# Kernel tuning notes

Measured on AMD Instinct MI355X. Metric: run time of the kernel, lower is better.

Reference implementation:

```python
import jax, jax.numpy as jnp
import numpy as np

B, S, C, H, W = 8, 20, 512, 48, 48
KC, VC, OC = 256, 512, 512

def conv1x1(x, w, b):
    # x: (B, Cin, H, W), w: (Cout, Cin), b: (Cout,)
    return jnp.einsum('oc,bchw->bohw', w, x) + b[None, :, None, None]

def setup_inputs() -> dict:
    key = jax.random.key(0)
    ks = jax.random.split(key, 16)
    sc = lambda cin: 1.0 / np.sqrt(cin)
    return {
        'key': jax.random.normal(ks[0], (B, C, H, W), jnp.float32),
        'query': jax.random.normal(ks[1], (B, S, C), jnp.float32),
        'word_id': jax.random.randint(ks[2], (B, S), 0, 1000),
        'wv_w': jax.random.normal(ks[3], (C, C), jnp.float32) * sc(C),
        'wv_b': jnp.zeros((C,), jnp.float32),
        'fk_w': jax.random.normal(ks[4], (KC, C), jnp.float32) * sc(C),
        'fk_b': jnp.zeros((KC,), jnp.float32),
        'fq_w': jax.random.normal(ks[5], (KC, C), jnp.float32) * sc(C),
        'fq_b': jnp.zeros((KC,), jnp.float32),
        'fv_w': jax.random.normal(ks[6], (VC, C), jnp.float32) * sc(C),
        'fv_b': jnp.zeros((VC,), jnp.float32),
        'w1_w': jax.random.normal(ks[7], (OC, 2 * C), jnp.float32) * sc(2 * C),
        'w1_b': jnp.zeros((OC,), jnp.float32),
        'w2_w': jax.random.normal(ks[8], (OC, C), jnp.float32) * sc(C),
        'w2_b': jnp.zeros((OC,), jnp.float32),
    }

def reference(key, query, word_id, wv_w, wv_b, fk_w, fk_b, fq_w, fq_b,
              fv_w, fv_b, w1_w, w1_b, w2_w, w2_b):
    b, c, h, w = key.shape
    hw = h * w
    # --- WordVisualAttention: context=query (B,S,C), visual=key ---
    vis = conv1x1(key, wv_w, wv_b).reshape(b, c, hw)          # (B,C,HW)
    attn = jnp.einsum('bsc,bcn->bsn', query, vis)             # (B,S,HW)
    attn = jax.nn.softmax(attn, axis=1)                       # softmax over seq dim
    mask = (word_id != 0).astype(attn.dtype)[:, :, None]      # (B,S,1)
    attn = attn * mask
    attn = attn / jnp.sum(attn, axis=1, keepdims=True)
    wemb = jnp.einsum('bsc,bsn->bcn', query, attn).reshape(b, c, h, w)
    # --- non-local cross attention ---
    k = conv1x1(key, fk_w, fk_b).reshape(b, KC, hw)           # (B,KC,HW)
    q = conv1x1(wemb, fq_w, fq_b).reshape(b, KC, hw)
    v = conv1x1(key, fv_w, fv_b).reshape(b, VC, hw)
    sim = jnp.einsum('bkn,bkm->bnm', q, k) * (KC ** -0.5)     # (B,HW,HW)
    sim = jax.nn.softmax(sim, axis=-1)
    ctx = jnp.einsum('bnm,bcm->bcn', sim, v).reshape(b, VC, h, w)
    out1 = conv1x1(jnp.concatenate([ctx, wemb], axis=1), w1_w, w1_b)
    out2 = conv1x1(ctx, w2_w, w2_b) + out1
    return out2
```

## Files before the change

### kernel.cpp

```cpp
#include <hip/hip_runtime.h>

#define NHW 2304
#define NB  8
#define NS  20
#define NC  512
#define SCL 0.09016844005555897f

typedef unsigned short u16;
typedef unsigned char u8;
typedef short short8 __attribute__((ext_vector_type(8)));
typedef unsigned short u16x8 __attribute__((ext_vector_type(8)));
typedef u8 u8x16 __attribute__((ext_vector_type(16)));
typedef float f32x4 __attribute__((ext_vector_type(4)));

__device__ __forceinline__ float b2f(u16 u) {
    unsigned int v = ((unsigned int)u) << 16;
    return __builtin_bit_cast(float, v);
}
__device__ __forceinline__ u16 f2b(float f) {
    unsigned int u = __builtin_bit_cast(unsigned int, f);
    u += 0x7fffu + ((u >> 16) & 1u);
    return (u16)(u >> 16);
}

__device__ __forceinline__ u8 f2e4_sw(float f) {
    unsigned int u = __builtin_bit_cast(unsigned int, f);
    u8 sign = (u >> 24) & 0x80;
    unsigned int a = u & 0x7FFFFFFFu;
    if (a >= 0x43E00000u) return sign | 0x7E;
    int e = (int)(a >> 23) - 127;
    unsigned int m = (a & 0x7FFFFF) | 0x800000;
    int ne = e + 7;
    if (ne <= 0) {
        int shift = 21 - ne;
        if (shift > 24) return sign;
        unsigned int q = m >> shift;
        unsigned int rem = m & ((1u << shift) - 1);
        unsigned int half = 1u << (shift - 1);
        q += (rem > half) || (rem == half && (q & 1));
        return sign | (u8)q;
    }
    unsigned int q = m >> 20;
    unsigned int rem = m & 0xFFFFFu;
    q += (rem > 0x80000u) || (rem == 0x80000u && (q & 1));
    if (q >= 16) { q >>= 1; ne++; }
    if (ne >= 16 || (ne == 15 && q == 15)) return sign | 0x7E;
    return sign | (u8)((ne << 3) | (q & 7));
}
__device__ __forceinline__ float e42f_sw(u8 v) {
    int e = (v >> 3) & 15;
    int m = v & 7;
    float r;
    if (e == 0) r = (float)m * 0.001953125f;
    else {
        unsigned int bits = ((unsigned int)(e + 120) << 23) | ((unsigned int)m << 20);
        r = __builtin_bit_cast(float, bits);
    }
    return (v & 0x80) ? -r : r;
}

#if defined(__has_builtin)
#if __has_builtin(__builtin_amdgcn_cvt_pk_fp8_f32) && __has_builtin(__builtin_amdgcn_cvt_f32_fp8)
#define HW_FP8 1
#endif
#endif

template<bool HI>
__device__ __forceinline__ unsigned int pk2_fp8(float a, float b, unsigned int old) {
#ifdef HW_FP8
    return (unsigned int)__builtin_amdgcn_cvt_pk_fp8_f32(a, b, (int)old, HI);
#else
    unsigned int lo = (unsigned int)f2e4_sw(a) | ((unsigned int)f2e4_sw(b) << 8);
    return HI ? ((old & 0x0000FFFFu) | (lo << 16)) : ((old & 0xFFFF0000u) | lo);
#endif
}
#ifdef HW_FP8
#define DEC_FP8(w, sel) __builtin_amdgcn_cvt_f32_fp8((int)(w), (sel))
#else
#define DEC_FP8(w, sel) e42f_sw((u8)((w) >> (8 * (sel))))
#endif

__device__ __forceinline__ void load_lds16(const void* g, void* l) {
    __builtin_amdgcn_global_load_lds((const __attribute__((address_space(1))) void*)g,
                                     (__attribute__((address_space(3))) void*)l, 16, 0, 0);
}

__global__ __launch_bounds__(256)
void gemm_nt_bf16(const u16* __restrict__ A, long As, int lda,
                  const u16* __restrict__ B, long Bs, int ldb,
                  void* __restrict__ C, long Cs, int ldc,
                  int K, const float* __restrict__ bias, int bias_mode,
                  float scale, int out_mode)
{
    __shared__ __align__(16) u16 sA[2 * 4096];
    __shared__ __align__(16) u16 sB[2 * 4096];
    const int tid   = threadIdx.x;
    const int b     = blockIdx.z;
    const int nBase = blockIdx.x * 128;
    const int mBase = blockIdx.y * 128;
    const u16* Ab = A + (size_t)b * As + (size_t)mBase * lda;
    const u16* Bb = B + (size_t)b * Bs + (size_t)nBase * ldb;
    const int lane = tid & 63;
    const int wave = tid >> 6;
    const int wr = wave >> 1, wc = wave & 1;
    const int srow[4] = { ((wave * 4 + 0) & 7) * 16 + (lane >> 2),
                          ((wave * 4 + 1) & 7) * 16 + (lane >> 2),
                          ((wave * 4 + 2) & 7) * 16 + (lane >> 2),
                          ((wave * 4 + 3) & 7) * 16 + (lane >> 2) };
    const int swzw = ((lane & 3) ^ ((lane >> 3) & 3)) * 8;
    const int rsw  = ((lane >> 4) ^ ((lane >> 1) & 3)) * 8;
    f32x4 acc[4][4] = {};
    for (int k0 = 0; k0 < K; k0 += 64) {
        __syncthreads();
        #pragma unroll
        for (int it = 0; it < 4; ++it) {
            const int chunk = wave * 4 + it;
            const int kofs = (chunk >> 3) * 32 + swzw;
            load_lds16(&Ab[(size_t)srow[it] * lda + k0 + kofs], &sA[chunk * 512 + lane * 8]);
            load_lds16(&Bb[(size_t)srow[it] * ldb + k0 + kofs], &sB[chunk * 512 + lane * 8]);
        }
        __syncthreads();
        #pragma unroll
        for (int kk = 0; kk < 2; ++kk) {
            short8 af[4], bg[4];
            #pragma unroll
            for (int i = 0; i < 4; ++i)
                af[i] = *(const short8*)&sA[kk * 4096 + (wr * 64 + i * 16 + (lane & 15)) * 32 + rsw];
            #pragma unroll
            for (int j = 0; j < 4; ++j)
                bg[j] = *(const short8*)&sB[kk * 4096 + (wc * 64 + j * 16 + (lane & 15)) * 32 + rsw];
            #pragma unroll
            for (int i = 0; i < 4; ++i)
                #pragma unroll
                for (int j = 0; j < 4; ++j)
                    acc[i][j] = __builtin_amdgcn_mfma_f32_16x16x32_bf16(af[i], bg[j], acc[i][j], 0, 0, 0);
        }
    }
    const int r0 = mBase + wr * 64 + (lane >> 4) * 4;
    const int c0 = nBase + wc * 64 + (lane & 15);
    #pragma unroll
    for (int i = 0; i < 4; ++i) {
        #pragma unroll
        for (int r = 0; r < 4; ++r) {
            const int row = r0 + i * 16 + r;
            const float br = (bias_mode == 1) ? bias[row] : 0.f;
            if (out_mode == 2) {
                float vv[4];
                #pragma unroll
                for (int j = 0; j < 4; ++j) vv[j] = acc[i][j][r] * scale + br;
                unsigned int w = 0;
                w = pk2_fp8<false>(vv[0], vv[1], w);
                w = pk2_fp8<true>(vv[2], vv[3], w);
                #pragma unroll
                for (int j = 0; j < 4; ++j)
                    ((u8*)C)[(size_t)b * Cs + (size_t)row * ldc + c0 + j * 16] = (u8)(w >> (8 * j));
            } else {
                #pragma unroll
                for (int j = 0; j < 4; ++j) {
                    const int col = c0 + j * 16;
                    float v = acc[i][j][r] * scale + br;
                    const size_t off = (size_t)b * Cs + (size_t)row * ldc + col;
                    if (out_mode == 1) ((float*)C)[off] = v;
                    else               ((u16*)C)[off] = f2b(v);
                }
            }
        }
    }
}

__global__ __launch_bounds__(256)
void e_gemm(const u16* __restrict__ attnwT, const u16* __restrict__ ks,
            u8* __restrict__ E8, float* __restrict__ Dpart)
{
    __shared__ __align__(16) u16 sA[128 * 32];
    __shared__ __align__(16) u16 sB[128 * 32];
    __shared__ __align__(16) u8 Etile[128 * 128];
    __shared__ float Dsh[2][128];
    const int tid = threadIdx.x;
    const int b = blockIdx.z;
    const int mt = blockIdx.x, nt = blockIdx.y;
    const int mBase = mt * 128, nBase = nt * 128;
    const u16* Ab = attnwT + ((size_t)b * NHW + nBase) * 32;
    const u16* Bb = ks     + ((size_t)b * NHW + mBase) * 32;
    const int lane = tid & 63;
    const int wave = tid >> 6;
    const int wr = wave >> 1, wc = wave & 1;
    const int str = tid >> 2;
    const int stk = (tid & 3) * 8;
    load_lds16(&Ab[(size_t)str * 32 + stk],        &sA[tid * 8]);
    load_lds16(&Ab[(size_t)(str + 64) * 32 + stk], &sA[2048 + tid * 8]);
    load_lds16(&Bb[(size_t)str * 32 + stk],        &sB[tid * 8]);
    load_lds16(&Bb[(size_t)(str + 64) * 32 + stk], &sB[2048 + tid * 8]);
    __syncthreads();
    short8 af[4], bg[4];
    #pragma unroll
    for (int i = 0; i < 4; ++i)
        af[i] = *(const short8*)&sA[(wr * 64 + i * 16 + (lane & 15)) * 32 + (lane >> 4) * 8];
    #pragma unroll
    for (int j = 0; j < 4; ++j)
        bg[j] = *(const short8*)&sB[(wc * 64 + j * 16 + (lane & 15)) * 32 + (lane >> 4) * 8];
    f32x4 acc[4][4] = {};
    #pragma unroll
    for (int i = 0; i < 4; ++i)
        #pragma unroll
        for (int j = 0; j < 4; ++j)
            acc[i][j] = __builtin_amdgcn_mfma_f32_16x16x32_bf16(af[i], bg[j], acc[i][j], 0, 0, 0);

    float dpart[16] = {};
    #pragma unroll
    for (int i = 0; i < 4; ++i) {
        #pragma unroll
        for (int r = 0; r < 4; ++r) {
            const int rowloc = wr * 64 + i * 16 + (lane >> 4) * 4 + r;
            unsigned int w = 0;
            w = pk2_fp8<false>(exp2f(acc[i][0][r]), exp2f(acc[i][1][r]), w);
            w = pk2_fp8<true>(exp2f(acc[i][2][r]), exp2f(acc[i][3][r]), w);
            dpart[i * 4 + r] += DEC_FP8(w, 0) + DEC_FP8(w, 1) + DEC_FP8(w, 2) + DEC_FP8(w, 3);
            #pragma unroll
            for (int j = 0; j < 4; ++j) {
                const int colloc = wc * 64 + j * 16 + (lane & 15);
                Etile[rowloc * 128 + (colloc ^ ((rowloc & 7) << 4))] = (u8)(w >> (8 * j));
            }
        }
    }
    #pragma unroll
    for (int mask = 1; mask < 16; mask <<= 1)
        #pragma unroll
        for (int k = 0; k < 16; ++k)
            dpart[k] += __shfl_xor(dpart[k], mask, 64);
    if ((lane & 15) == 0) {
        #pragma unroll
        for (int i = 0; i < 4; ++i)
            #pragma unroll
            for (int r = 0; r < 4; ++r)
                Dsh[wc][wr * 64 + i * 16 + (lane >> 4) * 4 + r] = dpart[i * 4 + r];
    }
    __syncthreads();
    if (tid < 128)
        Dpart[((size_t)(b * 18 + mt)) * NHW + nBase + tid] = Dsh[0][tid] + Dsh[1][tid];
    #pragma unroll
    for (int rep = 0; rep < 4; ++rep) {
        const int row = wave * 32 + rep * 8 + (lane >> 3);
        const int slot = lane & 7;
        u8x16 v = *(const u8x16*)&Etile[row * 128 + ((slot ^ (row & 7)) << 4)];
        *(u8x16*)&E8[((size_t)b * NHW + nBase + row) * NHW + mBase + slot * 16] = v;
    }
}

__global__ __launch_bounds__(256)
void pv_gemm(const u8* __restrict__ vp8, const u8* __restrict__ E8,
             const float* __restrict__ Dpart, const float* __restrict__ attnw,
             const float* __restrict__ Ofold, const float* __restrict__ b2,
             float* __restrict__ out)
{
    __shared__ __align__(16) u8 sA[16384];
    __shared__ __align__(16) u8 sB[16384];
    __shared__ float DsumSh[128];
    __shared__ float DinvSh[128];
    const int tid = threadIdx.x;
    const int bid = blockIdx.x;
    const int xcd = bid & 7, slot = bid >> 3;
    const int b = xcd;
    const int nt = slot >> 2;
    const int ot = slot & 3;
    const int oBase = ot * 128, nBase = nt * 128;

    const u8* A8 = vp8 + ((size_t)b * NC + oBase) * NHW;
    const u8* B8 = E8  + ((size_t)b * NHW + nBase) * NHW;
    const int lane = tid & 63;
    const int wave = tid >> 6;
    const int wr = wave >> 1, wc = wave & 1;

    int srowS[4], sgofS[4];
    #pragma unroll
    for (int it = 0; it < 4; ++it) {
        const int cd = (wave * 4 + it) * 64 + lane;
        srowS[it] = cd >> 3;
        sgofS[it] = ((cd & 7) ^ ((cd >> 3) & 7)) * 16;
    }
    #define PV_STAGE(k0) { \
        _Pragma("unroll") \
        for (int it = 0; it < 4; ++it) { \
            load_lds16(&A8[(size_t)srowS[it] * NHW + (k0) + sgofS[it]], &sA[((wave * 4 + it) * 64 + lane) * 16]); \
            load_lds16(&B8[(size_t)srowS[it] * NHW + (k0) + sgofS[it]], &sB[((wave * 4 + it) * 64 + lane) * 16]); \
        } }

    u16* sAh = (u16*)sA;
    u16* sBh = (u16*)sB;
    if (tid < 128) {
        float s = 0.f;
        #pragma unroll
        for (int mt = 0; mt < 18; ++mt)
            s += Dpart[((size_t)(b * 18 + mt)) * NHW + nBase + tid];
        DsumSh[tid] = s;
        DinvSh[tid] = 1.f / s;
    }
    for (int idx = tid; idx < 128 * 32; idx += 256) {
        const int o = idx >> 5, s = idx & 31;
        float v = 0.f;
        if (s < 20) v = Ofold[((size_t)b * 768 + 256 + oBase + o) * NS + s];
        else if (s == 20) v = b2[oBase + o];
        sAh[idx] = f2b(v);
    }
    __syncthreads();
    for (int idx = tid; idx < 128 * 32; idx += 256) {
        const int n = idx >> 5, s = idx & 31;
        float v = 0.f;
        if (s <= 20) {
            const float ds = DsumSh[n];
            v = (s < 20) ? attnw[((size_t)b * NS + s) * NHW + nBase + n] * ds : ds;
        }
        sBh[idx] = f2b(v);
    }
    __syncthreads();

    f32x4 acc[4][4];
    {
        const f32x4 zero = {0.f, 0.f, 0.f, 0.f};
        short8 qf[4], afr[4];
        #pragma unroll
        for (int i = 0; i < 4; ++i)
            qf[i] = *(const short8*)&sAh[(wr * 64 + i * 16 + (lane & 15)) * 32 + (lane >> 4) * 8];
        #pragma unroll
        for (int j = 0; j < 4; ++j)
            afr[j] = *(const short8*)&sBh[(wc * 64 + j * 16 + (lane & 15)) * 32 + (lane >> 4) * 8];
        #pragma unroll
        for (int i = 0; i < 4; ++i)
            #pragma unroll
            for (int j = 0; j < 4; ++j)
                acc[i][j] = __builtin_amdgcn_mfma_f32_16x16x32_bf16(qf[i], afr[j], zero, 0, 0, 0);
    }

    const int krow_a = wr * 64 + (lane & 15);
    const int krow_b = wc * 64 + (lane & 15);
    const int khalf = ((lane >> 4) & 1) * 8;
    const int kc2   = (lane >> 5);

    for (int k0 = 0; k0 < NHW; k0 += 128) {
        __syncthreads();
        PV_STAGE(k0);
        __syncthreads();
        #pragma unroll
        for (int kk = 0; kk < 4; ++kk) {
            long af[4], bg[4];
            #pragma unroll
            for (int i = 0; i < 4; ++i) {
                const int row = krow_a + i * 16;
                const int c = (kk * 2 + kc2) ^ (row & 7);
                af[i] = *(const long*)&sA[row * 128 + c * 16 + khalf];
            }
            #pragma unroll
            for (int j = 0; j < 4; ++j) {
                const int row = krow_b + j * 16;
                const int c = (kk * 2 + kc2) ^ (row & 7);
                bg[j] = *(const long*)&sB[row * 128 + c * 16 + khalf];
            }
            #pragma unroll
            for (int i = 0; i < 4; ++i)
                #pragma unroll
                for (int j = 0; j < 4; ++j)
                    acc[i][j] = __builtin_amdgcn_mfma_f32_16x16x32_fp8_fp8(af[i], bg[j], acc[i][j], 0, 0, 0);
        }
    }
    #pragma unroll
    for (int i = 0; i < 4; ++i) {
        #pragma unroll
        for (int r = 0; r < 4; ++r) {
            const int rowloc = wr * 64 + i * 16 + (lane >> 4) * 4 + r;
            #pragma unroll
            for (int j = 0; j < 4; ++j) {
                const int colloc = wc * 64 + j * 16 + (lane & 15);
                out[((size_t)b * NC + oBase + rowloc) * NHW + nBase + colloc] =
                    acc[i][j][r] * DinvSh[colloc];
            }
        }
    }
    #undef PV_STAGE
}

__global__ __launch_bounds__(256)
void prep_all(const float* __restrict__ key, u16* __restrict__ keyT,
              const float* __restrict__ fv_w, u16* __restrict__ fvT,
              const float* __restrict__ w1, const float* __restrict__ w1b,
              const float* __restrict__ w2, const float* __restrict__ w2b,
              const float* __restrict__ fvb, u16* __restrict__ wc2b,
              float* __restrict__ b2,
              const float* __restrict__ query, const float* __restrict__ wv_w,
              const float* __restrict__ wv_b, float* __restrict__ qw,
              float* __restrict__ qb,
              const float* __restrict__ fq, float* __restrict__ O)
{
    __shared__ __align__(16) char smem[44032];
    const int bid = blockIdx.x;
    const int tid = threadIdx.x;

    if (bid < 2368) {
        const float* src; u16* dst; int R, Cc, cBase, rBase, b;
        if (bid < 2304) {
            src = key; dst = keyT; R = NC; Cc = NHW;
            cBase = (bid % 36) * 64; rBase = ((bid / 36) % 8) * 64; b = bid / 288;
        } else {
            const int t2 = bid - 2304;
            src = fv_w; dst = fvT; R = 512; Cc = 512;
            cBase = (t2 % 8) * 64; rBase = (t2 / 8) * 64; b = 0;
        }
        u16 (*t)[72] = (u16(*)[72])smem;
        const float* sb = src + ((size_t)b * R + rBase) * Cc + cBase;
        const int ln = tid & 63;
        const int lr = tid >> 6;
        #pragma unroll
        for (int rr = 0; rr < 16; ++rr) {
            int r = lr + rr * 4;
            t[r][ln] = f2b(sb[(size_t)r * Cc + ln]);
        }
        __syncthreads();
        u16* ob = dst + ((size_t)b * Cc + cBase) * R + rBase;
        #pragma unroll
        for (int rep = 0; rep < 2; ++rep) {
            int slot = rep * 256 + tid;
            int cc = slot >> 3;
            int r8 = (slot & 7) * 8;
            u16x8 v;
            #pragma unroll
            for (int e = 0; e < 8; ++e) v[e] = t[r8 + e][cc];
            *(u16x8*)&ob[(size_t)cc * R + r8] = v;
        }
    } else if (bid < 2880) {
        const int o = bid - 2368;
        float* red = (float*)smem;
        float part = 0.f;
        for (int c = tid; c < 512; c += 256) {
            float v = w1[(size_t)o * 1024 + c] + w2[(size_t)o * 512 + c];
            wc2b[(size_t)o * 512 + c] = f2b(v);
            part += v * fvb[c];
        }
        #pragma unroll
        for (int off = 32; off > 0; off >>= 1) part += __shfl_down(part, off, 64);
        if ((tid & 63) == 0) red[tid >> 6] = part;
        __syncthreads();
        if (tid == 0) b2[o] = (red[0] + red[1]) + (red[2] + red[3]) + w1b[o] + w2b[o];
    } else if (bid < 3040) {
        const int t3 = bid - 2880;
        const int s = t3 % NS, b = t3 / NS;
        float* qs  = (float*)smem;
        float* red = qs + 512;
        qs[tid] = query[((size_t)b * NS + s) * NC + tid];
        qs[tid + 256] = query[((size_t)b * NS + s) * NC + tid + 256];
        __syncthreads();
        float a0 = 0.f, a1 = 0.f;
        for (int o = 0; o < NC; ++o) {
            float qv = qs[o];
            a0 += qv * wv_w[(size_t)o * NC + tid];
            a1 += qv * wv_w[(size_t)o * NC + tid + 256];
        }
        qw[((size_t)b * NS + s) * NC + tid] = a0;
        qw[((size_t)b * NS + s) * NC + tid + 256] = a1;
        float pb = qs[tid] * wv_b[tid] + qs[tid + 256] * wv_b[tid + 256];
        #pragma unroll
        for (int off = 32; off > 0; off >>= 1) pb += __shfl_down(pb, off, 64);
        if ((tid & 63) == 0) red[tid >> 6] = pb;
        __syncthreads();
        if (tid == 0) qb[b * NS + s] = (red[0] + red[1]) + (red[2] + red[3]);
    } else {
        const int t4 = bid - 3040;
        const int x = t4 % 48, b = t4 / 48;
        float (*qsh)[NC] = (float(*)[NC])smem;
        for (int idx = tid; idx < NS * NC; idx += 256)
            qsh[idx >> 9][idx & 511] = query[(size_t)b * NS * NC + idx];
        __syncthreads();
        const int row = x * 16 + (tid >> 4);
        const int ct = tid & 15;
        const float* wp = (row < 256) ? &fq[(size_t)row * NC]
                                      : &w1[(size_t)(row - 256) * 1024 + 512];
        float acc[NS] = {};
        #pragma unroll 4
        for (int i = 0; i < 32; ++i) {
            int c = ct + i * 16;
            float w = wp[c];
            #pragma unroll
            for (int s = 0; s < NS; ++s) acc[s] += w * qsh[s][c];
        }
        #pragma unroll
        for (int off = 1; off < 16; off <<= 1)
            #pragma unroll
            for (int s = 0; s < NS; ++s) acc[s] += __shfl_xor(acc[s], off, 64);
        if (ct == 0) {
            #pragma unroll
            for (int s = 0; s < NS; ++s)
                O[((size_t)b * 768 + row) * NS + s] = acc[s];
        }
    }
}

__global__ __launch_bounds__(256)
void scan_wk(const float* __restrict__ key, const float* __restrict__ qw,
             const float* __restrict__ qb, const int* __restrict__ wid,
             const float* __restrict__ g, const float* __restrict__ h,
             float* __restrict__ attnw, u16* __restrict__ attnwT,
             u16* __restrict__ ks)
{
    __shared__ float qshT[NC][20];
    __shared__ u16 gshb[NC][22];
    __shared__ float red[3][64][7];
    __shared__ float msk[20], qbs[20], hsh[21];
    const int b = blockIdx.y;
    const int tid = threadIdx.x;
    const float* qwb = qw + (size_t)b * NS * NC;
    for (int idx = tid; idx < NC * 20; idx += 256) {
        int c = idx / 20, s = idx - c * 20;
        qshT[c][s] = qwb[s * NC + c];
    }
    for (int idx = tid; idx < NC * 21; idx += 256) {
        int c = idx / 21, s = idx - c * 21;
        gshb[c][s] = f2b(g[((size_t)b * NC + c) * 24 + s]);
    }
    if (tid < 20) {
        msk[tid] = (wid[b * NS + tid] != 0) ? 1.f : 0.f;
        qbs[tid] = qb[b * NS + tid];
    }
    if (tid < 21) hsh[tid] = h[b * 24 + tid];
    __syncthreads();
    const int wave = tid >> 6, lane = tid & 63;
    const int n = blockIdx.x * 64 + lane;
    const int cbase = wave * 128;
    const float* kp = key + (size_t)b * NC * NHW + n;
    float acc[41];
    #pragma unroll
    for (int s = 0; s < 41; ++s)
        acc[s] = (wave == 0) ? (s < 20 ? qbs[s] : hsh[s - 20]) : 0.f;
    #pragma unroll 4
    for (int ci = 0; ci < 128; ++ci) {
        const int c = cbase + ci;
        float kv = kp[(size_t)c * NHW];
        #pragma unroll
        for (int s = 0; s < 20; ++s) acc[s] += qshT[c][s] * kv;
        #pragma unroll
        for (int s = 0; s < 21; ++s) acc[20 + s] += b2f(gshb[c][s]) * kv;
    }
    #pragma unroll
    for (int r = 0; r < 6; ++r) {
        if (wave > 0) {
            #pragma unroll
            for (int k = 0; k < 7; ++k) {
                int idx = r * 7 + k;
                if (idx < 41) red[wave - 1][lane][k] = acc[idx];
            }
        }
        __syncthreads();
        if (wave == 0) {
            #pragma unroll
            for (int k = 0; k < 7; ++k) {
                int idx = r * 7 + k;
                if (idx < 41)
                    acc[idx] += red[0][lane][k] + red[1][lane][k] + red[2][lane][k];
            }
        }
        __syncthreads();
    }
    if (wave == 0) {
        float mx = acc[0];
        #pragma unroll
        for (int s = 1; s < 20; ++s) mx = fmaxf(mx, acc[s]);
        float msum = 0.f;
        #pragma unroll
        for (int s = 0; s < 20; ++s) {
            acc[s] = __expf(acc[s] - mx) * msk[s];
            msum += acc[s];
        }
        const float rr = 1.f / msum;
        u16 row32[32];
        #pragma unroll
        for (int s = 0; s < 20; ++s) {
            float a = acc[s] * rr;
            attnw[((size_t)b * NS + s) * NHW + n] = a;
            row32[s] = f2b(a);
        }
        row32[20] = 0x3F80;
        #pragma unroll
        for (int s = 21; s < 32; ++s) row32[s] = 0;
        u16* dp = attnwT + ((size_t)b * NHW + n) * 32;
        #pragma unroll
        for (int q = 0; q < 4; ++q)
            *(u16x8*)&dp[q * 8] = *(u16x8*)&row32[q * 8];
        u16 rk[32];
        #pragma unroll
        for (int s = 0; s < 21; ++s) rk[s] = f2b(acc[20 + s]);
        #pragma unroll
        for (int s = 21; s < 32; ++s) rk[s] = 0;
        u16* kp2 = ks + ((size_t)b * NHW + n) * 32;
        #pragma unroll
        for (int q = 0; q < 4; ++q)
            *(u16x8*)&kp2[q * 8] = *(u16x8*)&rk[q * 8];
    }
}

__global__ __launch_bounds__(256)
void fold_g(const float* __restrict__ O, const float* __restrict__ fk,
            const float* __restrict__ fq_b, const float* __restrict__ fk_b,
            float* __restrict__ g, float* __restrict__ h)
{
    __shared__ float fqqsh[256][21];
    __shared__ float fqbsh[256];
    __shared__ float red[3][64][7];
    const int b = blockIdx.y;
    const int tid = threadIdx.x;
    for (int idx = tid; idx < 256 * NS; idx += 256) {
        int kc = idx / NS, s = idx - kc * NS;
        fqqsh[kc][s] = O[((size_t)b * 768 + kc) * NS + s];
    }
    fqbsh[tid] = fq_b[tid];
    __syncthreads();
    const int wave = tid >> 6, lane = tid & 63;
    const int c = blockIdx.x * 64 + lane;
    float acc[21] = {};
    for (int i = 0; i < 64; ++i) {
        int kc = wave * 64 + i;
        float w = fk[(size_t)kc * NC + c];
        #pragma unroll
        for (int s = 0; s < NS; ++s) acc[s] += w * fqqsh[kc][s];
        acc[20] += w * fqbsh[kc];
    }
    #pragma unroll
    for (int r = 0; r < 3; ++r) {
        if (wave > 0) {
            #pragma unroll
            for (int k = 0; k < 7; ++k) red[wave - 1][lane][k] = acc[r * 7 + k];
        }
        __syncthreads();
        if (wave == 0) {
            #pragma unroll
            for (int k = 0; k < 7; ++k)
                acc[r * 7 + k] += red[0][lane][k] + red[1][lane][k] + red[2][lane][k];
        }
        __syncthreads();
    }
    if (wave == 0) {
        float* gp = &g[((size_t)b * NC + c) * 24];
        #pragma unroll
        for (int s = 0; s < 21; ++s) gp[s] = acc[s] * SCL;
        gp[21] = gp[22] = gp[23] = 0.f;
    }
    if (blockIdx.x == 0 && tid < 21) {
        float hh = 0.f;
        for (int kc = 0; kc < 256; ++kc)
            hh += fk_b[kc] * (tid < 20 ? fqqsh[kc][tid] : fqbsh[kc]);
        h[b * 24 + tid] = hh * SCL;
    }
}

extern "C" void kernel_launch(void* const* d_in, const int* in_sizes, int n_in,
                              void* d_out, int out_size, void* d_ws, size_t ws_size,
                              hipStream_t stream)
{
    const float* key   = (const float*)d_in[0];
    const float* query = (const float*)d_in[1];
    const int*   wid   = (const int*)d_in[2];
    const float* wv_w  = (const float*)d_in[3];
    const float* wv_b  = (const float*)d_in[4];
    const float* fk_w  = (const float*)d_in[5];
    const float* fk_b  = (const float*)d_in[6];
    const float* fq_w  = (const float*)d_in[7];
    const float* fq_b  = (const float*)d_in[8];
    const float* fv_w  = (const float*)d_in[9];
    const float* fv_b  = (const float*)d_in[10];
    const float* w1_w  = (const float*)d_in[11];
    const float* w1_b  = (const float*)d_in[12];
    const float* w2_w  = (const float*)d_in[13];
    const float* w2_b  = (const float*)d_in[14];
    float* out = (float*)d_out;

    char* p = (char*)d_ws;
    u16*   keyT   = (u16*)p;   p += (size_t)NB * NHW * NC * 2;
    u8*    E8     = (u8*)p;    p += (size_t)NB * NHW * NHW;
    u8*    vp8    = (u8*)p;    p += (size_t)NB * NC * NHW;
    u16*   fvT    = (u16*)p;   p += (size_t)512 * 512 * 2;
    u16*   wc2b   = (u16*)p;   p += (size_t)512 * 512 * 2;
    u16*   wcv    = (u16*)p;   p += (size_t)512 * 512 * 2;
    u16*   attnwT = (u16*)p;   p += (size_t)NB * NHW * 32 * 2;
    u16*   ksb    = (u16*)p;   p += (size_t)NB * NHW * 32 * 2;
    float* attnw  = (float*)p; p += (size_t)NB * NS * NHW * 4;
    float* qw     = (float*)p; p += (size_t)NB * NS * NC * 4;
    float* qbuf   = (float*)p; p += (size_t)NB * NS * 4;
    float* Ofold  = (float*)p; p += (size_t)NB * 768 * NS * 4;
    float* g      = (float*)p; p += (size_t)NB * NC * 24 * 4;
    float* h      = (float*)p; p += (size_t)NB * 24 * 4;
    float* b2     = (float*)p; p += (size_t)512 * 4;
    float* Dpart  = (float*)p; p += (size_t)NB * 18 * NHW * 4;

    dim3 blk(256);

    prep_all<<<dim3(3424), blk, 0, stream>>>(
        key, keyT, fv_w, fvT, w1_w, w1_b, w2_w, w2_b, fv_b, wc2b, b2,
        query, wv_w, wv_b, qw, qbuf, fq_w, Ofold);
    fold_g<<<dim3(8, NB), blk, 0, stream>>>(Ofold, fk_w, fq_b, fk_b, g, h);
    scan_wk<<<dim3(36, NB), blk, 0, stream>>>(key, qw, qbuf, wid, g, h,
                                              attnw, attnwT, ksb);

    gemm_nt_bf16<<<dim3(4, 4, 1), blk, 0, stream>>>(
        wc2b, 0, 512, fvT, 0, 512, wcv, 0, 512, 512,
        nullptr, 0, 1.f, 0);
    gemm_nt_bf16<<<dim3(18, 4, NB), blk, 0, stream>>>(
        wcv, 0, 512, keyT, (long)NHW * 512, 512,
        vp8, (long)NC * NHW, NHW, 512,
        nullptr, 0, 1.f, 2);
    e_gemm<<<dim3(18, 18, NB), blk, 0, stream>>>(attnwT, ksb, E8, Dpart);
    pv_gemm<<<dim3(576), blk, 0, stream>>>(vp8, E8, Dpart, attnw, Ofold, b2, out);
}
```

Before: 215.3 us.

## Merge independent kernels into two heterogeneous launches to overlap small stages

Combines fold_g with the weight-combine GEMM into one launch, and the scan/softmax kernel with the V-projection GEMM into another, dispatching work by block index. This removes two kernel launches and lets independent, under-filled stages share the GPU concurrently. The cost is that all blocks in the merged kernel reserve the larger shared-memory footprint, which can reduce occupancy for the GEMM blocks. The GEMM body is also refactored into a device function and its unused bias/fp32 output paths are dropped.

```diff
diff --git a/kernel.cpp b/kernel.cpp
--- a/kernel.cpp
+++ b/kernel.cpp
@@ -85,21 +85,12 @@
                                      (__attribute__((address_space(3))) void*)l, 16, 0, 0);
 }
 
-__global__ __launch_bounds__(256)
-void gemm_nt_bf16(const u16* __restrict__ A, long As, int lda,
-                  const u16* __restrict__ B, long Bs, int ldb,
-                  void* __restrict__ C, long Cs, int ldc,
-                  int K, const float* __restrict__ bias, int bias_mode,
-                  float scale, int out_mode)
+__device__ __forceinline__ void gemm_body(
+    const u16* __restrict__ Ab, int lda, const u16* __restrict__ Bb, int ldb,
+    void* __restrict__ Cb, int ldc, int K, float scale, int out_mode,
+    int mBase, int nBase, u16* sA, u16* sB)
 {
-    __shared__ __align__(16) u16 sA[2 * 4096];
-    __shared__ __align__(16) u16 sB[2 * 4096];
-    const int tid   = threadIdx.x;
-    const int b     = blockIdx.z;
-    const int nBase = blockIdx.x * 128;
-    const int mBase = blockIdx.y * 128;
-    const u16* Ab = A + (size_t)b * As + (size_t)mBase * lda;
-    const u16* Bb = B + (size_t)b * Bs + (size_t)nBase * ldb;
+    const int tid = threadIdx.x;
     const int lane = tid & 63;
     const int wave = tid >> 6;
     const int wr = wave >> 1, wc = wave & 1;
@@ -143,26 +134,20 @@
         #pragma unroll
         for (int r = 0; r < 4; ++r) {
             const int row = r0 + i * 16 + r;
-            const float br = (bias_mode == 1) ? bias[row] : 0.f;
             if (out_mode == 2) {
                 float vv[4];
                 #pragma unroll
-                for (int j = 0; j < 4; ++j) vv[j] = acc[i][j][r] * scale + br;
+                for (int j = 0; j < 4; ++j) vv[j] = acc[i][j][r] * scale;
                 unsigned int w = 0;
                 w = pk2_fp8<false>(vv[0], vv[1], w);
                 w = pk2_fp8<true>(vv[2], vv[3], w);
                 #pragma unroll
                 for (int j = 0; j < 4; ++j)
-                    ((u8*)C)[(size_t)b * Cs + (size_t)row * ldc + c0 + j * 16] = (u8)(w >> (8 * j));
+                    ((u8*)Cb)[(size_t)row * ldc + c0 + j * 16] = (u8)(w >> (8 * j));
             } else {
                 #pragma unroll
-                for (int j = 0; j < 4; ++j) {
-                    const int col = c0 + j * 16;
-                    float v = acc[i][j][r] * scale + br;
-                    const size_t off = (size_t)b * Cs + (size_t)row * ldc + col;
-                    if (out_mode == 1) ((float*)C)[off] = v;
-                    else               ((u16*)C)[off] = f2b(v);
-                }
+                for (int j = 0; j < 4; ++j)
+                    ((u16*)Cb)[(size_t)row * ldc + c0 + j * 16] = f2b(acc[i][j][r] * scale);
             }
         }
     }
@@ -493,158 +478,191 @@
 }
 
 __global__ __launch_bounds__(256)
-void scan_wk(const float* __restrict__ key, const float* __restrict__ qw,
-             const float* __restrict__ qb, const int* __restrict__ wid,
-             const float* __restrict__ g, const float* __restrict__ h,
-             float* __restrict__ attnw, u16* __restrict__ attnwT,
-             u16* __restrict__ ks)
+void mid_all(const float* __restrict__ O, const float* __restrict__ fk,
+             const float* __restrict__ fq_b, const float* __restrict__ fk_b,
+             float* __restrict__ g, float* __restrict__ h,
+             const u16* __restrict__ wc2b, const u16* __restrict__ fvT,
+             u16* __restrict__ wcv)
 {
-    __shared__ float qshT[NC][20];
-    __shared__ u16 gshb[NC][22];
-    __shared__ float red[3][64][7];
-    __shared__ float msk[20], qbs[20], hsh[21];
-    const int b = blockIdx.y;
+    __shared__ __align__(16) char smem[32768];
+    const int bid = blockIdx.x;
     const int tid = threadIdx.x;
-    const float* qwb = qw + (size_t)b * NS * NC;
-    for (int idx = tid; idx < NC * 20; idx += 256) {
-        int c = idx / 20, s = idx - c * 20;
-        qshT[c][s] = qwb[s * NC + c];
-    }
-    for (int idx = tid; idx < NC * 21; idx += 256) {
-        int c = idx / 21, s = idx - c * 21;
-        gshb[c][s] = f2b(g[((size_t)b * NC + c) * 24 + s]);
-    }
-    if (tid < 20) {
-        msk[tid] = (wid[b * NS + tid] != 0) ? 1.f : 0.f;
-        qbs[tid] = qb[b * NS + tid];
-    }
-    if (tid < 21) hsh[tid] = h[b * 24 + tid];
-    __syncthreads();
-    const int wave = tid >> 6, lane = tid & 63;
-    const int n = blockIdx.x * 64 + lane;
-    const int cbase = wave * 128;
-    const float* kp = key + (size_t)b * NC * NHW + n;
-    float acc[41];
-    #pragma unroll
-    for (int s = 0; s < 41; ++s)
-        acc[s] = (wave == 0) ? (s < 20 ? qbs[s] : hsh[s - 20]) : 0.f;
-    #pragma unroll 4
-    for (int ci = 0; ci < 128; ++ci) {
-        const int c = cbase + ci;
-        float kv = kp[(size_t)c * NHW];
-        #pragma unroll
-        for (int s = 0; s < 20; ++s) acc[s] += qshT[c][s] * kv;
-        #pragma unroll
-        for (int s = 0; s < 21; ++s) acc[20 + s] += b2f(gshb[c][s]) * kv;
-    }
-    #pragma unroll
-    for (int r = 0; r < 6; ++r) {
-        if (wave > 0) {
-            #pragma unroll
-            for (int k = 0; k < 7; ++k) {
-                int idx = r * 7 + k;
-                if (idx < 41) red[wave - 1][lane][k] = acc[idx];
-            }
-        }
-        __syncthreads();
+    if (bid < 64) {
+        const int xb = bid & 7, b = bid >> 3;
+        float (*fqqsh)[21] = (float(*)[21])smem;
+        float* fqbsh = (float*)(smem + 21504);
+        float (*red)[64][7] = (float(*)[64][7])(smem + 22528);
+        for (int idx = tid; idx < 256 * NS; idx += 256) {
+            int kc = idx / NS, s = idx - kc * NS;
+            fqqsh[kc][s] = O[((size_t)b * 768 + kc) * NS + s];
+        }
+        fqbsh[tid] = fq_b[tid];
+        __syncthreads();
+        const int wave = tid >> 6, lane = tid & 63;
+        const int c = xb * 64 + lane;
+        float acc[21] = {};
+        for (int i = 0; i < 64; ++i) {
+            int kc = wave * 64 + i;
+            float w = fk[(size_t)kc * NC + c];
+            #pragma unroll
+            for (int s = 0; s < NS; ++s) acc[s] += w * fqqsh[kc][s];
+            acc[20] += w * fqbsh[kc];
+        }
+        #pragma unroll
+        for (int r = 0; r < 3; ++r) {
+            if (wave > 0) {
+                #pragma unroll
+                for (int k = 0; k < 7; ++k) red[wave - 1][lane][k] = acc[r * 7 + k];
+            }
+            __syncthreads();
+            if (wave == 0) {
+                #pragma unroll
+                for (int k = 0; k < 7; ++k)
+                    acc[r * 7 + k] += red[0][lane][k] + red[1][lane][k] + red[2][lane][k];
+            }
+            __syncthreads();
+        }
         if (wave == 0) {
-            #pragma unroll
-            for (int k = 0; k < 7; ++k) {
-                int idx = r * 7 + k;
-                if (idx < 41)
-                    acc[idx] += red[0][lane][k] + red[1][lane][k] + red[2][lane][k];
-            }
-        }
-        __syncthreads();
-    }
-    if (wave == 0) {
-        float mx = acc[0];
-        #pragma unroll
-        for (int s = 1; s < 20; ++s) mx = fmaxf(mx, acc[s]);
-        float msum = 0.f;
-        #pragma unroll
-        for (int s = 0; s < 20; ++s) {
-            acc[s] = __expf(acc[s] - mx) * msk[s];
-            msum += acc[s];
-        }
-        const float rr = 1.f / msum;
-        u16 row32[32];
-        #pragma unroll
-        for (int s = 0; s < 20; ++s) {
-            float a = acc[s] * rr;
-            attnw[((size_t)b * NS + s) * NHW + n] = a;
-            row32[s] = f2b(a);
-        }
-        row32[20] = 0x3F80;
-        #pragma unroll
-        for (int s = 21; s < 32; ++s) row32[s] = 0;
-        u16* dp = attnwT + ((size_t)b * NHW + n) * 32;
-        #pragma unroll
-        for (int q = 0; q < 4; ++q)
-            *(u16x8*)&dp[q * 8] = *(u16x8*)&row32[q * 8];
-        u16 rk[32];
-        #pragma unroll
-        for (int s = 0; s < 21; ++s) rk[s] = f2b(acc[20 + s]);
-        #pragma unroll
-        for (int s = 21; s < 32; ++s) rk[s] = 0;
-        u16* kp2 = ks + ((size_t)b * NHW + n) * 32;
-        #pragma unroll
-        for (int q = 0; q < 4; ++q)
-            *(u16x8*)&kp2[q * 8] = *(u16x8*)&rk[q * 8];
+            float* gp = &g[((size_t)b * NC + c) * 24];
+            #pragma unroll
+            for (int s = 0; s < 21; ++s) gp[s] = acc[s] * SCL;
+            gp[21] = gp[22] = gp[23] = 0.f;
+        }
+        if (xb == 0 && tid < 21) {
+            float hh = 0.f;
+            for (int kc = 0; kc < 256; ++kc)
+                hh += fk_b[kc] * (tid < 20 ? fqqsh[kc][tid] : fqbsh[kc]);
+            h[b * 24 + tid] = hh * SCL;
+        }
+    } else {
+        const int t = bid - 64;
+        const int nBase = (t & 3) * 128;
+        const int mBase = (t >> 2) * 128;
+        u16* sA = (u16*)smem;
+        u16* sB = (u16*)(smem + 16384);
+        gemm_body(wc2b + (size_t)mBase * 512, 512, fvT + (size_t)nBase * 512, 512,
+                  wcv, 512, 512, 1.f, 0, mBase, nBase, sA, sB);
     }
 }
 
 __global__ __launch_bounds__(256)
-void fold_g(const float* __restrict__ O, const float* __restrict__ fk,
-            const float* __restrict__ fq_b, const float* __restrict__ fk_b,
-            float* __restrict__ g, float* __restrict__ h)
+void scan_vproj(const float* __restrict__ key, const float* __restrict__ qw,
+                const float* __restrict__ qb, const int* __restrict__ wid,
+                const float* __restrict__ g, const float* __restrict__ h,
+                float* __restrict__ attnw, u16* __restrict__ attnwT,
+                u16* __restrict__ ks,
+                const u16* __restrict__ wcv, const u16* __restrict__ keyT,
+                u8* __restrict__ vp8)
 {
-    __shared__ float fqqsh[256][21];
-    __shared__ float fqbsh[256];
-    __shared__ float red[3][64][7];
-    const int b = blockIdx.y;
+    __shared__ __align__(16) char smem[69632];
+    const int bid = blockIdx.x;
     const int tid = threadIdx.x;
-    for (int idx = tid; idx < 256 * NS; idx += 256) {
-        int kc = idx / NS, s = idx - kc * NS;
-        fqqsh[kc][s] = O[((size_t)b * 768 + kc) * NS + s];
-    }
-    fqbsh[tid] = fq_b[tid];
-    __syncthreads();
-    const int wave = tid >> 6, lane = tid & 63;
-    const int c = blockIdx.x * 64 + lane;
-    float acc[21] = {};
-    for (int i = 0; i < 64; ++i) {
-        int kc = wave * 64 + i;
-        float w = fk[(size_t)kc * NC + c];
-        #pragma unroll
-        for (int s = 0; s < NS; ++s) acc[s] += w * fqqsh[kc][s];
-        acc[20] += w * fqbsh[kc];
-    }
-    #pragma unroll
-    for (int r = 0; r < 3; ++r) {
-        if (wave > 0) {
-            #pragma unroll
-            for (int k = 0; k < 7; ++k) red[wave - 1][lane][k] = acc[r * 7 + k];
-        }
-        __syncthreads();
+    if (bid < 288) {
+        const int xb = bid % 36, b = bid / 36;
+        float (*qshT)[20] = (float(*)[20])smem;
+        u16 (*gshb)[22] = (u16(*)[22])(smem + 40960);
+        float (*red)[64][7] = (float(*)[64][7])(smem + 63488);
+        float* msk = (float*)(smem + 68864);
+        float* qbs = (float*)(smem + 68944);
+        float* hsh = (float*)(smem + 69024);
+        const float* qwb = qw + (size_t)b * NS * NC;
+        for (int idx = tid; idx < NC * 20; idx += 256) {
+            int c = idx / 20, s = idx - c * 20;
+            qshT[c][s] = qwb[s * NC + c];
+        }
+        for (int idx = tid; idx < NC * 21; idx += 256) {
+            int c = idx / 21, s = idx - c * 21;
+            gshb[c][s] = f2b(g[((size_t)b * NC + c) * 24 + s]);
+        }
+        if (tid < 20) {
+            msk[tid] = (wid[b * NS + tid] != 0) ? 1.f : 0.f;
+            qbs[tid] = qb[b * NS + tid];
+        }
+        if (tid < 21) hsh[tid] = h[b * 24 + tid];
+        __syncthreads();
+        const int wave = tid >> 6, lane = tid & 63;
+        const int n = xb * 64 + lane;
+        const int cbase = wave * 128;
+        const float* kp = key + (size_t)b * NC * NHW + n;
+        float acc[41];
+        #pragma unroll
+        for (int s = 0; s < 41; ++s)
+            acc[s] = (wave == 0) ? (s < 20 ? qbs[s] : hsh[s - 20]) : 0.f;
+        #pragma unroll 4
+        for (int ci = 0; ci < 128; ++ci) {
+            const int c = cbase + ci;
+            float kv = kp[(size_t)c * NHW];
+            #pragma unroll
+            for (int s = 0; s < 20; ++s) acc[s] += qshT[c][s] * kv;
+            #pragma unroll
+            for (int s = 0; s < 21; ++s) acc[20 + s] += b2f(gshb[c][s]) * kv;
+        }
+        #pragma unroll
+        for (int r = 0; r < 6; ++r) {
+            if (wave > 0) {
+                #pragma unroll
+                for (int k = 0; k < 7; ++k) {
+                    int idx = r * 7 + k;
+                    if (idx < 41) red[wave - 1][lane][k] = acc[idx];
+                }
+            }
+            __syncthreads();
+            if (wave == 0) {
+                #pragma unroll
+                for (int k = 0; k < 7; ++k) {
+                    int idx = r * 7 + k;
+                    if (idx < 41)
+                        acc[idx] += red[0][lane][k] + red[1][lane][k] + red[2][lane][k];
+                }
+            }
+            __syncthreads();
+        }
         if (wave == 0) {
-            #pragma unroll
-            for (int k = 0; k < 7; ++k)
-                acc[r * 7 + k] += red[0][lane][k] + red[1][lane][k] + red[2][lane][k];
-        }
-        __syncthreads();
-    }
-    if (wave == 0) {
-        float* gp = &g[((size_t)b * NC + c) * 24];
-        #pragma unroll
-        for (int s = 0; s < 21; ++s) gp[s] = acc[s] * SCL;
-        gp[21] = gp[22] = gp[23] = 0.f;
-    }
-    if (blockIdx.x == 0 && tid < 21) {
-        float hh = 0.f;
-        for (int kc = 0; kc < 256; ++kc)
-            hh += fk_b[kc] * (tid < 20 ? fqqsh[kc][tid] : fqbsh[kc]);
-        h[b * 24 + tid] = hh * SCL;
+            float mx = acc[0];
+            #pragma unroll
+            for (int s = 1; s < 20; ++s) mx = fmaxf(mx, acc[s]);
+            float msum = 0.f;
+            #pragma unroll
+            for (int s = 0; s < 20; ++s) {
+                acc[s] = __expf(acc[s] - mx) * msk[s];
+                msum += acc[s];
+            }
+            const float rr = 1.f / msum;
+            u16 row32[32];
+            #pragma unroll
+            for (int s = 0; s < 20; ++s) {
+                float a = acc[s] * rr;
+                attnw[((size_t)b * NS + s) * NHW + n] = a;
+                row32[s] = f2b(a);
+            }
+            row32[20] = 0x3F80;
+            #pragma unroll
+            for (int s = 21; s < 32; ++s) row32[s] = 0;
+            u16* dp = attnwT + ((size_t)b * NHW + n) * 32;
+            #pragma unroll
+            for (int q = 0; q < 4; ++q)
+                *(u16x8*)&dp[q * 8] = *(u16x8*)&row32[q * 8];
+            u16 rk[32];
+            #pragma unroll
+            for (int s = 0; s < 21; ++s) rk[s] = f2b(acc[20 + s]);
+            #pragma unroll
+            for (int s = 21; s < 32; ++s) rk[s] = 0;
+            u16* kp2 = ks + ((size_t)b * NHW + n) * 32;
+            #pragma unroll
+            for (int q = 0; q < 4; ++q)
+                *(u16x8*)&kp2[q * 8] = *(u16x8*)&rk[q * 8];
+        }
+    } else {
+        const int t = bid - 288;
+        const int nBase = (t % 18) * 128;
+        const int mBase = ((t / 18) & 3) * 128;
+        const int bb = t / 72;
+        u16* sA = (u16*)smem;
+        u16* sB = (u16*)(smem + 16384);
+        gemm_body(wcv + (size_t)mBase * 512, 512,
+                  keyT + (size_t)bb * NHW * 512 + (size_t)nBase * 512, 512,
+                  vp8 + (size_t)bb * NC * NHW, NHW, 512, 1.f, 2,
+                  mBase, nBase, sA, sB);
     }
 }
 
@@ -692,17 +710,10 @@
     prep_all<<<dim3(3424), blk, 0, stream>>>(
         key, keyT, fv_w, fvT, w1_w, w1_b, w2_w, w2_b, fv_b, wc2b, b2,
         query, wv_w, wv_b, qw, qbuf, fq_w, Ofold);
-    fold_g<<<dim3(8, NB), blk, 0, stream>>>(Ofold, fk_w, fq_b, fk_b, g, h);
-    scan_wk<<<dim3(36, NB), blk, 0, stream>>>(key, qw, qbuf, wid, g, h,
-                                              attnw, attnwT, ksb);
-
-    gemm_nt_bf16<<<dim3(4, 4, 1), blk, 0, stream>>>(
-        wc2b, 0, 512, fvT, 0, 512, wcv, 0, 512, 512,
-        nullptr, 0, 1.f, 0);
-    gemm_nt_bf16<<<dim3(18, 4, NB), blk, 0, stream>>>(
-        wcv, 0, 512, keyT, (long)NHW * 512, 512,
-        vp8, (long)NC * NHW, NHW, 512,
-        nullptr, 0, 1.f, 2);
+    mid_all<<<dim3(80), blk, 0, stream>>>(
+        Ofold, fk_w, fq_b, fk_b, g, h, wc2b, fvT, wcv);
+    scan_vproj<<<dim3(864), blk, 0, stream>>>(
+        key, qw, qbuf, wid, g, h, attnw, attnwT, ksb, wcv, keyT, vp8);
     e_gemm<<<dim3(18, 18, NB), blk, 0, stream>>>(attnwT, ksb, E8, Dpart);
     pv_gemm<<<dim3(576), blk, 0, stream>>>(vp8, E8, Dpart, attnw, Ofold, b2, out);
 }
```

Result: faster. 202.6 us (-5.9%).
